# Optimization experiments

Hardware: AMD Instinct MI355X
Metric: run time of the kernel (lower is better)

The kernel has to match this reference:

```python
import jax, jax.numpy as jnp
import numpy as np

N_USERS = 60000
N_ITEMS = 40000
D = 64
N_BEH = 3
L_GLOBAL = 2
L_SINGLE = 2
E_GLOBAL = 1_000_000
E_BEH = 500_000
BATCH = 4096
REG_WEIGHT = 1e-3
DIM_QK = 64
N_NODES = N_USERS + 1 + N_ITEMS + 1
USER_GLOBAL_W = 2.35
USER_BEH_W = 0.242
ITEM_GLOBAL_W = 1.0
ITEM_BEH_W = 0.55


def setup_inputs() -> dict:
    key = jax.random.key(0)
    ks = jax.random.split(key, 9)
    user_emb = (jax.random.normal(ks[0], (N_USERS + 1, D), jnp.float32) * 0.1).at[0].set(0.0)
    item_emb = (jax.random.normal(ks[1], (N_ITEMS + 1, D), jnp.float32) * 0.1).at[0].set(0.0)
    w_scale = 1.0 / np.sqrt(D)
    global_W = jax.random.normal(ks[2], (L_GLOBAL, D, D), jnp.float32) * w_scale
    global_b = jnp.zeros((L_GLOBAL, D), jnp.float32)
    beh_W = jax.random.normal(ks[3], (N_BEH, L_SINGLE, D, D), jnp.float32) * w_scale
    beh_b = jnp.zeros((N_BEH, L_SINGLE, D), jnp.float32)
    all_edge_index = jax.random.randint(ks[4], (2, E_GLOBAL), 0, N_NODES, jnp.int32)
    beh_edge_index = jax.random.randint(ks[5], (N_BEH, 2, E_BEH), 0, N_NODES, jnp.int32)
    batch_data = jax.random.randint(ks[6], (BATCH, N_BEH, 3), 0, N_ITEMS + 1, jnp.int32)
    return {
        "user_emb": user_emb, "item_emb": item_emb,
        "global_W": global_W, "global_b": global_b,
        "beh_W": beh_W, "beh_b": beh_b,
        "all_edge_index": all_edge_index, "beh_edge_index": beh_edge_index,
        "batch_data": batch_data,
    }


def _gcn_conv(h, src, dst, W, b):
    # PyG GCNConv, add_self_loops=False: out[dst] += d^-1/2[src] d^-1/2[dst] (h W)[src] + b
    N = h.shape[0]
    hw = h @ W
    deg = jnp.zeros((N,), hw.dtype).at[dst].add(1.0)
    dinv = jnp.where(deg > 0, jax.lax.rsqrt(jnp.maximum(deg, 1.0)), 0.0)
    coef = (dinv[src] * dinv[dst])[:, None]          # [E,1]
    out = jax.ops.segment_sum(hw[src] * coef, dst, num_segments=N)
    return out + b


def _graph_encoder(x, edge_index, Ws, bs):
    src, dst = edge_index[0], edge_index[1]
    res = x
    h = x
    for i in range(Ws.shape[0]):
        h = _gcn_conv(h, src, dst, Ws[i], bs[i])
        h = h / jnp.maximum(jnp.linalg.norm(h, axis=-1, keepdims=True), 1e-12)  # F.normalize
        res = res + h / (i + 1.0)
    return res


def _mutual_attention(tok):
    # tok: [N, B, D]; per-node BxB softmax attention
    scale = 1.0 / np.sqrt(DIM_QK)
    att = jax.nn.softmax(jnp.einsum('nbd,ncd->nbc', tok, tok) * scale, axis=-1)
    return jnp.einsum('nbc,ncd->nbd', att, tok)


def reference(user_emb, item_emb, global_W, global_b, beh_W, beh_b,
              all_edge_index, beh_edge_index, batch_data):
    nu = user_emb.shape[0]
    all_emb = jnp.concatenate([user_emb, item_emb], axis=0)        # [N, D]
    all_emb = _graph_encoder(all_emb, all_edge_index, global_W, global_b)
    u_g, i_g = all_emb[:nu], all_emb[nu:]
    beh_u, beh_i = [], []
    for b_idx in range(N_BEH):
        e = _graph_encoder(all_emb, beh_edge_index[b_idx], beh_W[b_idx], beh_b[b_idx])
        beh_u.append(e[:nu])
        beh_i.append(e[nu:])
    all_u = jnp.stack(beh_u, axis=1)                               # [nu, B, D]
    all_i = jnp.stack(beh_i, axis=1)                               # [ni, B, D]
    all_u = _mutual_attention(all_u)
    all_i = _mutual_attention(all_i)
    uw = USER_GLOBAL_W * u_g[:, None, :] + USER_BEH_W * all_u      # [nu, B, D]
    iw = ITEM_GLOBAL_W * i_g[:, None, :] + ITEM_BEH_W * all_i      # [ni, B, D]

    total = jnp.float32(0.0)
    for i in range(N_BEH):
        data = batch_data[:, i]
        users = data[:, 0]
        items = data[:, 1:]                                        # [batch, 2]
        uf = uw[:, i][users][:, None, :]                           # [batch, 1, D]
        for j in range(N_BEH):
            itf = iw[:, j][items]                                  # [batch, 2, D]
            scores = jnp.sum(uf * itf, axis=2)                     # [batch, 2]
            total = total - jnp.mean(jax.nn.log_sigmoid(scores[:, 0] - scores[:, 1]))
    emb_loss = (jnp.linalg.norm(user_emb) + jnp.linalg.norm(item_emb)) / item_emb.shape[0]
    return total + REG_WEIGHT * emb_loss
```

## Files before the change

### kernel.cpp

```cpp
#include <hip/hip_runtime.h>
#include <math.h>

#define NU 60001
#define NI 40001
#define NN 100002
#define EG 1000000
#define EB 500000
#define BATCH 4096
#define NPASS 4
#define PASSW 25001
#define EC 36
#define SENTB (NN * 64)

typedef float floatx2 __attribute__((ext_vector_type(2)));
typedef short bf16x8 __attribute__((ext_vector_type(8)));
typedef float f32x4 __attribute__((ext_vector_type(4)));

__device__ inline float wave_sum(float v) {
#pragma unroll
  for (int off = 32; off > 0; off >>= 1) v += __shfl_down(v, off);
  return __shfl(v, 0);
}

__device__ inline float sub_sum16(float v) {
#pragma unroll
  for (int off = 8; off > 0; off >>= 1) v += __shfl_xor(v, off);
  return v;
}

__device__ inline float dot4(float4 a, float4 b) {
  return fmaf(a.x, b.x, fmaf(a.y, b.y, fmaf(a.z, b.z, a.w * b.w)));
}

__device__ inline unsigned short f2b(float f) {
  unsigned u = __float_as_uint(f);
  return (unsigned short)((u + 0x7fffu + ((u >> 16) & 1u)) >> 16);
}
__device__ inline float b2f(unsigned short h) {
  return __uint_as_float((unsigned)h << 16);
}
__device__ inline float4 ld4b(const unsigned short* p) {
  ushort4 u = *(const ushort4*)p;
  return make_float4(b2f(u.x), b2f(u.y), b2f(u.z), b2f(u.w));
}
__device__ inline unsigned pack2b(float a, float b) {
  return (unsigned)f2b(a) | ((unsigned)f2b(b) << 16);
}

__device__ inline unsigned char f2fp8(float f) {
  return (unsigned char)(__builtin_amdgcn_cvt_pk_fp8_f32(f, f, 0, false) & 0xff);
}
__device__ inline unsigned int pack4_fp8(float4 v) {
  int pk = __builtin_amdgcn_cvt_pk_fp8_f32(v.x, v.y, 0, false);
  pk = __builtin_amdgcn_cvt_pk_fp8_f32(v.z, v.w, pk, true);
  return (unsigned int)pk;
}

__global__ void k_bucket(const int* __restrict__ eg, const int* __restrict__ eb,
                         int* __restrict__ cnt, int* __restrict__ edg,
                         int lo, int hi) {
  int set = blockIdx.y;
  int E = set ? EB : EG;
  int e = blockIdx.x * blockDim.x + threadIdx.x;
  if (e >= E) return;
  const int* sp = set ? (eb + (long)(set - 1) * 2 * EB) : eg;
  int d = sp[E + e];
  if (d < lo || d >= hi) return;
  int s = sp[e];
  int pos = atomicAdd(cnt + set * NN + d, 1);
  if (pos < EC) edg[((long)set * NN + d) * EC + pos] = s << 6;
}

__global__ void k_dinv(const int* __restrict__ cnt, float* __restrict__ dinv) {
  int i = blockIdx.x * blockDim.x + threadIdx.x;
  if (i < 4 * NN) {
    int c = cnt[i];
    dinv[i] = (c > 0) ? rsqrtf((float)c) : 0.f;
  }
}

__global__ void k_prepw(const float* __restrict__ gW, const float* __restrict__ bW,
                        unsigned short* __restrict__ wt) {
  int t = blockIdx.x * blockDim.x + threadIdx.x;
  if (t >= 8 * 4096) return;
  int m = t >> 12, idx = t & 4095;
  int col = idx >> 6, k = idx & 63;
  const float* src = (m < 2) ? (gW + m * 4096) : (bW + (long)(m - 2) * 4096);
  wt[t] = f2b(src[k * 64 + col]);
}

__global__ void k_zsent(unsigned char* __restrict__ tbsb, unsigned char* __restrict__ asg,
                        unsigned char* __restrict__ asb) {
  const long NEp = (long)(NN + 1) * 64;
  int t = threadIdx.x;
  int row = t >> 6, b = t & 63;
  if (row < 3) tbsb[row * NEp + SENTB + b] = 0;
  else if (row == 3) asg[SENTB + b] = 0;
  else if (row < 7) asb[(row - 4) * NEp + SENTB + b] = 0;
}

__global__ void k_tbs0(const float4* __restrict__ ue, const float4* __restrict__ ie,
                       const float* __restrict__ dinv, unsigned int* __restrict__ out) {
  long i = (long)blockIdx.x * blockDim.x + threadIdx.x;
  if (i >= (long)(NN + 1) * 16) return;
  int row = (int)(i >> 4);
  if (row >= NN) { out[i] = 0; return; }
  float4 v = (row < NU) ? ue[i] : ie[i - (long)NU * 16];
  float dv = dinv[row];
  v.x *= dv; v.y *= dv; v.z *= dv; v.w *= dv;
  out[i] = pack4_fp8(v);
}

#define CVT8(r)                                       \
  a0 += __builtin_amdgcn_cvt_pk_f32_fp8(r.x, false);  \
  a1 += __builtin_amdgcn_cvt_pk_f32_fp8(r.x, true);   \
  a2 += __builtin_amdgcn_cvt_pk_f32_fp8(r.y, false);  \
  a3 += __builtin_amdgcn_cvt_pk_f32_fp8(r.y, true);

template <int MODE>
__global__ void __launch_bounds__(256) k_gcn(
    const unsigned char* __restrict__ tb, const int* __restrict__ edg,
    const int* __restrict__ cnt, const float* __restrict__ dinv,
    const unsigned short* __restrict__ Wt, const float* __restrict__ biasb,
    const float* __restrict__ basef, const float* __restrict__ base2f,
    const unsigned short* __restrict__ base16,
    unsigned short* __restrict__ res16, unsigned char* __restrict__ outS,
    unsigned char* __restrict__ tbs123) {
  __shared__ __align__(16) short accs[32][72];
  __shared__ float ssq[32][2];
  const long NE = (long)NN * 64;
  const long NEp = (long)(NN + 1) * 64;

  int t = threadIdx.x;
  int w = t >> 6, lane = t & 63;
  int sub3 = lane >> 3, sl8 = lane & 7;
  int sub = lane >> 4, sl16 = lane & 15;
  int set = blockIdx.y;

  const float* bias;
  if (MODE <= 1) bias = biasb;
  else bias = biasb + set * 128 + (MODE == 3 ? 64 : 0);
  const unsigned short* wt = Wt + ((MODE >= 2) ? (long)set * 8192 : 0);
  int cs = (MODE >= 2) ? (1 + set) : 0;
  const unsigned char* tbl = (MODE >= 2) ? tb + (long)set * NEp : tb;
  unsigned char* outp = (MODE == 2) ? outS + (long)set * NEp : outS;

  int tilebase = (w >> 1) << 4;
  int cg = (w & 1) << 5;
  int ncolA = cg + sl16, ncolB = cg + 16 + sl16;
  bf16x8 bfA0 = *(const bf16x8*)(wt + ncolA * 64 + (sub << 3));
  bf16x8 bfA1 = *(const bf16x8*)(wt + ncolA * 64 + 32 + (sub << 3));
  bf16x8 bfB0 = *(const bf16x8*)(wt + ncolB * 64 + (sub << 3));
  bf16x8 bfB1 = *(const bf16x8*)(wt + ncolB * 64 + 32 + (sub << 3));
  float biasA = bias[ncolA], biasB = bias[ncolB];

  int nb0 = blockIdx.x * 32;
  int node = nb0 + (w << 3) + sub3;
  floatx2 a0 = {0.f, 0.f}, a1 = {0.f, 0.f}, a2 = {0.f, 0.f}, a3 = {0.f, 0.f};
  int deg = 0;
  float dvn = 0.f;
  const int* ep = edg;
  if (node < NN) {
    deg = min(cnt[cs * NN + node], EC);
    dvn = dinv[cs * NN + node];
    ep = edg + ((long)cs * NN + node) * EC;
  }
  int mx = deg;
  mx = max(mx, __shfl_xor(mx, 8));
  mx = max(mx, __shfl_xor(mx, 16));
  mx = max(mx, __shfl_xor(mx, 32));
  for (int ch = 0; ch < mx; ch += 8) {
    int rem = deg - ch;
#pragma unroll
    for (int i = 0; i < 8; i += 4) {
      int s0 = ep[ch + i + 0];
      int s1 = ep[ch + i + 1];
      int s2 = ep[ch + i + 2];
      int s3 = ep[ch + i + 3];
      int o0 = (i + 0 < rem) ? s0 : SENTB;
      int o1 = (i + 1 < rem) ? s1 : SENTB;
      int o2 = (i + 2 < rem) ? s2 : SENTB;
      int o3 = (i + 3 < rem) ? s3 : SENTB;
      uint2 r0 = *(const uint2*)(tbl + o0 + (sl8 << 3));
      uint2 r1 = *(const uint2*)(tbl + o1 + (sl8 << 3));
      uint2 r2 = *(const uint2*)(tbl + o2 + (sl8 << 3));
      uint2 r3 = *(const uint2*)(tbl + o3 + (sl8 << 3));
      CVT8(r0); CVT8(r1); CVT8(r2); CVT8(r3);
    }
  }
  floatx2 dv2 = {dvn, dvn};
  a0 *= dv2; a1 *= dv2; a2 *= dv2; a3 *= dv2;
  int4 pk4;
  pk4.x = (int)pack2b(a0.x, a0.y);
  pk4.y = (int)pack2b(a1.x, a1.y);
  pk4.z = (int)pack2b(a2.x, a2.y);
  pk4.w = (int)pack2b(a3.x, a3.y);
  *(int4*)&accs[(w << 3) + sub3][sl8 << 3] = pk4;
  __syncthreads();

  int arow = tilebase + sl16;
  bf16x8 fa0 = *(const bf16x8*)&accs[arow][sub << 3];
  bf16x8 fa1 = *(const bf16x8*)&accs[arow][32 + (sub << 3)];
  f32x4 cA = {0.f, 0.f, 0.f, 0.f}, cB = {0.f, 0.f, 0.f, 0.f};
  cA = __builtin_amdgcn_mfma_f32_16x16x32_bf16(fa0, bfA0, cA, 0, 0, 0);
  cA = __builtin_amdgcn_mfma_f32_16x16x32_bf16(fa1, bfA1, cA, 0, 0, 0);
  cB = __builtin_amdgcn_mfma_f32_16x16x32_bf16(fa0, bfB0, cB, 0, 0, 0);
  cB = __builtin_amdgcn_mfma_f32_16x16x32_bf16(fa1, bfB1, cB, 0, 0, 0);

  float vA[4], vB[4];
#pragma unroll
  for (int r = 0; r < 4; r++) { vA[r] = cA[r] + biasA; vB[r] = cB[r] + biasB; }
#pragma unroll
  for (int r = 0; r < 4; r++) {
    float p = sub_sum16(fmaf(vA[r], vA[r], vB[r] * vB[r]));
    if (sl16 == 0) ssq[tilebase + (sub << 2) + r][w & 1] = p;
  }
  __syncthreads();
#pragma unroll
  for (int r = 0; r < 4; r++) {
    int nl = tilebase + (sub << 2) + r;
    float ss = ssq[nl][0] + ssq[nl][1];
    float inv = 1.0f / fmaxf(sqrtf(ss), 1e-12f);
    float hA = vA[r] * inv, hB = vB[r] * inv;
    int gn = nb0 + nl;
    if (gn < NN) {
      long iA = (long)gn * 64 + ncolA, iB = (long)gn * 64 + ncolB;
      float dv = dinv[cs * NN + gn];
      if (MODE == 0 || MODE == 2) {
        outp[iA] = f2fp8(hA * dv);
        outp[iB] = f2fp8(hB * dv);
      } else if (MODE == 1) {
        float idv = (dv > 0.f) ? 1.0f / dv : 0.f;
        float ownA = __builtin_amdgcn_cvt_f32_fp8((unsigned int)tbl[iA], 0) * idv;
        float ownB = __builtin_amdgcn_cvt_f32_fp8((unsigned int)tbl[iB], 0) * idv;
        float bA, bB;
        if (gn < NU) { bA = basef[iA]; bB = basef[iB]; }
        else {
          long o2 = (long)(gn - NU) * 64;
          bA = base2f[o2 + ncolA]; bB = base2f[o2 + ncolB];
        }
        float rA = bA + ownA + 0.5f * hA, rB = bB + ownB + 0.5f * hB;
        res16[iA] = f2b(rA); res16[iB] = f2b(rB);
#pragma unroll
        for (int k = 0; k < 3; k++) {
          float dk = dinv[(1 + k) * NN + gn];
          tbs123[(long)k * NEp + iA] = f2fp8(rA * dk);
          tbs123[(long)k * NEp + iB] = f2fp8(rB * dk);
        }
      } else {
        float idv = (dv > 0.f) ? 1.0f / dv : 0.f;
        float ownA = __builtin_amdgcn_cvt_f32_fp8((unsigned int)tbl[iA], 0) * idv;
        float ownB = __builtin_amdgcn_cvt_f32_fp8((unsigned int)tbl[iB], 0) * idv;
        float rA = b2f(base16[iA]) + ownA + 0.5f * hA;
        float rB = b2f(base16[iB]) + ownB + 0.5f * hB;
        (res16 + (long)set * NE)[iA] = f2b(rA);
        (res16 + (long)set * NE)[iB] = f2b(rB);
      }
    }
  }
}

__device__ inline void item_iw4(const unsigned short* __restrict__ G,
                                const unsigned short* __restrict__ B0,
                                const unsigned short* __restrict__ B1,
                                const unsigned short* __restrict__ B2,
                                long o, float4& iw0, float4& iw1, float4& iw2) {
  float4 g = ld4b(G + o);
  float4 t0 = ld4b(B0 + o);
  float4 t1 = ld4b(B1 + o);
  float4 t2 = ld4b(B2 + o);
  float g00 = sub_sum16(dot4(t0, t0)), g01 = sub_sum16(dot4(t0, t1));
  float g02 = sub_sum16(dot4(t0, t2)), g11 = sub_sum16(dot4(t1, t1));
  float g12 = sub_sum16(dot4(t1, t2)), g22 = sub_sum16(dot4(t2, t2));
  const float S = 0.125f;
  float gm[3][3] = {{g00, g01, g02}, {g01, g11, g12}, {g02, g12, g22}};
  float4* out[3] = {&iw0, &iw1, &iw2};
#pragma unroll
  for (int j = 0; j < 3; j++) {
    float a0 = gm[j][0] * S, a1 = gm[j][1] * S, a2 = gm[j][2] * S;
    float m = fmaxf(a0, fmaxf(a1, a2));
    float e0 = expf(a0 - m), e1 = expf(a1 - m), e2 = expf(a2 - m);
    float inv = 1.f / (e0 + e1 + e2);
    float w0 = e0 * inv, w1 = e1 * inv, w2 = e2 * inv;
    float4 r;
    r.x = fmaf(0.55f, w0 * t0.x + w1 * t1.x + w2 * t2.x, g.x);
    r.y = fmaf(0.55f, w0 * t0.y + w1 * t1.y + w2 * t2.y, g.y);
    r.z = fmaf(0.55f, w0 * t0.z + w1 * t1.z + w2 * t2.z, g.z);
    r.w = fmaf(0.55f, w0 * t0.w + w1 * t1.w + w2 * t2.w, g.w);
    *out[j] = r;
  }
}

__global__ void __launch_bounds__(256) k_loss(
    const unsigned short* __restrict__ G, const unsigned short* __restrict__ B0,
    const unsigned short* __restrict__ B1, const unsigned short* __restrict__ B2,
    const int* __restrict__ batch, float* __restrict__ acc) {
  int tid = blockIdx.x * blockDim.x + threadIdx.x;
  int lane = tid & 63;
  int sub = lane >> 4, sl = lane & 15;
  int task = (tid >> 6) * 4 + sub;
  if (task >= BATCH * 3) return;
  int i = task % 3;
  const int* bd = batch + (long)task * 3;
  int u = bd[0], p = bd[1], q = bd[2];

  float4 uf;
  {
    long o = (long)u * 64 + sl * 4;
    float4 g = ld4b(G + o);
    float4 t0 = ld4b(B0 + o);
    float4 t1 = ld4b(B1 + o);
    float4 t2 = ld4b(B2 + o);
    float4 ti = (i == 0) ? t0 : ((i == 1) ? t1 : t2);
    float a0 = sub_sum16(dot4(ti, t0)) * 0.125f;
    float a1 = sub_sum16(dot4(ti, t1)) * 0.125f;
    float a2 = sub_sum16(dot4(ti, t2)) * 0.125f;
    float m = fmaxf(a0, fmaxf(a1, a2));
    float e0 = expf(a0 - m), e1 = expf(a1 - m), e2 = expf(a2 - m);
    float inv = 1.f / (e0 + e1 + e2);
    float w0 = e0 * inv, w1 = e1 * inv, w2 = e2 * inv;
    uf.x = fmaf(2.35f, g.x, 0.242f * (w0 * t0.x + w1 * t1.x + w2 * t2.x));
    uf.y = fmaf(2.35f, g.y, 0.242f * (w0 * t0.y + w1 * t1.y + w2 * t2.y));
    uf.z = fmaf(2.35f, g.z, 0.242f * (w0 * t0.z + w1 * t1.z + w2 * t2.z));
    uf.w = fmaf(2.35f, g.w, 0.242f * (w0 * t0.w + w1 * t1.w + w2 * t2.w));
  }

  float4 p0, p1, p2, q0, q1, q2;
  item_iw4(G, B0, B1, B2, ((long)(NU + p)) * 64 + sl * 4, p0, p1, p2);
  item_iw4(G, B0, B1, B2, ((long)(NU + q)) * 64 + sl * 4, q0, q1, q2);

  float sp0 = sub_sum16(dot4(uf, p0)), sq0 = sub_sum16(dot4(uf, q0));
  float sp1 = sub_sum16(dot4(uf, p1)), sq1 = sub_sum16(dot4(uf, q1));
  float sp2 = sub_sum16(dot4(uf, p2)), sq2 = sub_sum16(dot4(uf, q2));

  if (sl == 0) {
    float loc = 0.f;
    float xs[3] = {sp0 - sq0, sp1 - sq1, sp2 - sq2};
#pragma unroll
    for (int j = 0; j < 3; j++) {
      float x = xs[j];
      loc += fminf(x, 0.f) - log1pf(expf(-fabsf(x)));
    }
    atomicAdd(acc, loc);
  }
}

__global__ void k_sumsq(const float* __restrict__ x, long n, float* __restrict__ acc) {
  long stride = (long)gridDim.x * blockDim.x;
  float v = 0.f;
  for (long i = (long)blockIdx.x * blockDim.x + threadIdx.x; i < n; i += stride) {
    float t = x[i];
    v = fmaf(t, t, v);
  }
  v = wave_sum(v);
  if ((threadIdx.x & 63) == 0) atomicAdd(acc, v);
}

__global__ void k_final(const float* __restrict__ acc, float* __restrict__ out) {
  out[0] = -acc[0] * (1.0f / (float)BATCH) +
           0.001f * ((sqrtf(acc[1]) + sqrtf(acc[2])) / (float)NI);
}

extern "C" void kernel_launch(void* const* d_in, const int* in_sizes, int n_in,
                              void* d_out, int out_size, void* d_ws, size_t ws_size,
                              hipStream_t stream) {
  const float* ue = (const float*)d_in[0];
  const float* ie = (const float*)d_in[1];
  const float* gW = (const float*)d_in[2];
  const float* gb = (const float*)d_in[3];
  const float* bW = (const float*)d_in[4];
  const float* bb = (const float*)d_in[5];
  const int* eg = (const int*)d_in[6];
  const int* eb = (const int*)d_in[7];
  const int* batch = (const int*)d_in[8];
  float* out = (float*)d_out;

  const long NE = (long)NN * 64;
  const long NEp = (long)(NN + 1) * 64;
  unsigned short* G16 = (unsigned short*)d_ws;
  unsigned short* B16 = G16 + NE;
  float* DINV = (float*)(B16 + 3 * NE);
  float* ACC = DINV + 4 * NN;
  int* CNT = (int*)(ACC + 8);
  unsigned short* WT = (unsigned short*)(CNT + 4 * NN);
  int* EDG = (int*)(WT + 8 * 4096);
  unsigned char* TBS0 = (unsigned char*)(EDG + 4L * NN * EC);
  unsigned char* TBSb = TBS0 + NEp;
  unsigned char* ASg = TBSb + 3 * NEp;
  unsigned char* ASb = ASg + NEp;

  hipMemsetAsync(ACC, 0, 8 * sizeof(float), stream);
  hipMemsetAsync(CNT, 0, 4 * NN * sizeof(int), stream);

  const int GB = (NN + 31) / 32;

  dim3 ge((EG + 255) / 256, 4);

  for (int p = 0; p < NPASS; p++)
    k_bucket<<<ge, 256, 0, stream>>>(eg, eb, CNT, EDG,
                                     p * PASSW, min(NN, (p + 1) * PASSW));
  k_dinv<<<(4 * NN + 255) / 256, 256, 0, stream>>>(CNT, DINV);

  k_prepw<<<128, 256, 0, stream>>>(gW, bW, WT);

  k_zsent<<<1, 512, 0, stream>>>(TBSb, ASg, ASb);
  k_tbs0<<<(int)(((NN + 1) * 16 + 255) / 256), 256, 0, stream>>>(
      (const float4*)ue, (const float4*)ie, DINV, (unsigned int*)TBS0);

  k_gcn<0><<<dim3(GB, 1), 256, 0, stream>>>(TBS0, EDG, CNT, DINV, WT, gb,
                                            nullptr, nullptr, nullptr, nullptr,
                                            ASg, nullptr);
  k_gcn<1><<<dim3(GB, 1), 256, 0, stream>>>(ASg, EDG, CNT, DINV, WT + 4096,
                                            gb + 64, ue, ie, nullptr, G16,
                                            nullptr, TBSb);

  k_gcn<2><<<dim3(GB, 3), 256, 0, stream>>>(TBSb, EDG, CNT, DINV, WT + 8192,
                                            bb, nullptr, nullptr, nullptr,
                                            nullptr, ASb, nullptr);
  k_gcn<3><<<dim3(GB, 3), 256, 0, stream>>>(ASb, EDG, CNT, DINV, WT + 12288,
                                            bb, nullptr, nullptr, G16, B16,
                                            nullptr, nullptr);

  k_loss<<<(BATCH * 3) / 16, 256, 0, stream>>>(G16, B16, B16 + NE, B16 + 2 * NE,
                                               batch, ACC);

  k_sumsq<<<512, 256, 0, stream>>>(ue, (long)NU * 64, ACC + 1);
  k_sumsq<<<512, 256, 0, stream>>>(ie, (long)NI * 64, ACC + 2);

  k_final<<<1, 1, 0, stream>>>(ACC, out);
}
```

Measured before the change: 533.9 us.

## Prefetch first 16 edges per node, split accumulators, fuse prep kernels

Merges the dinv, weight-prep and sentinel-zeroing kernels into one launch. The GCN gather kernel now loads the first 16 edge indices as int4 vectors and issues 16 independent neighbour gathers at once, with two accumulator sets to raise memory-level parallelism. Weight and bias fragment loads move after the gather to ease register pressure, and launch bounds now request 8 blocks per CU. Nodes with low degree still pay for the 16 sentinel loads, and the occupancy hint may cause register spills.

```diff
diff --git a/kernel.cpp b/kernel.cpp
--- a/kernel.cpp
+++ b/kernel.cpp
@@ -71,32 +71,29 @@
   if (pos < EC) edg[((long)set * NN + d) * EC + pos] = s << 6;
 }
 
-__global__ void k_dinv(const int* __restrict__ cnt, float* __restrict__ dinv) {
+__global__ void k_prep(const int* __restrict__ cnt, float* __restrict__ dinv,
+                       const float* __restrict__ gW, const float* __restrict__ bW,
+                       unsigned short* __restrict__ wt,
+                       unsigned char* __restrict__ tbsb, unsigned char* __restrict__ asg,
+                       unsigned char* __restrict__ asb) {
+  const long NEp = (long)(NN + 1) * 64;
   int i = blockIdx.x * blockDim.x + threadIdx.x;
   if (i < 4 * NN) {
     int c = cnt[i];
     dinv[i] = (c > 0) ? rsqrtf((float)c) : 0.f;
   }
-}
-
-__global__ void k_prepw(const float* __restrict__ gW, const float* __restrict__ bW,
-                        unsigned short* __restrict__ wt) {
-  int t = blockIdx.x * blockDim.x + threadIdx.x;
-  if (t >= 8 * 4096) return;
-  int m = t >> 12, idx = t & 4095;
-  int col = idx >> 6, k = idx & 63;
-  const float* src = (m < 2) ? (gW + m * 4096) : (bW + (long)(m - 2) * 4096);
-  wt[t] = f2b(src[k * 64 + col]);
-}
-
-__global__ void k_zsent(unsigned char* __restrict__ tbsb, unsigned char* __restrict__ asg,
-                        unsigned char* __restrict__ asb) {
-  const long NEp = (long)(NN + 1) * 64;
-  int t = threadIdx.x;
-  int row = t >> 6, b = t & 63;
-  if (row < 3) tbsb[row * NEp + SENTB + b] = 0;
-  else if (row == 3) asg[SENTB + b] = 0;
-  else if (row < 7) asb[(row - 4) * NEp + SENTB + b] = 0;
+  if (i < 8 * 4096) {
+    int m = i >> 12, idx = i & 4095;
+    int col = idx >> 6, k = idx & 63;
+    const float* src = (m < 2) ? (gW + m * 4096) : (bW + (long)(m - 2) * 4096);
+    wt[i] = f2b(src[k * 64 + col]);
+  }
+  if (i < 448) {
+    int row = i >> 6, b = i & 63;
+    if (row < 3) tbsb[row * NEp + SENTB + b] = 0;
+    else if (row == 3) asg[SENTB + b] = 0;
+    else asb[(row - 4) * NEp + SENTB + b] = 0;
+  }
 }
 
 __global__ void k_tbs0(const float4* __restrict__ ue, const float4* __restrict__ ie,
@@ -111,14 +108,20 @@
   out[i] = pack4_fp8(v);
 }
 
-#define CVT8(r)                                       \
+#define CVTA(r)                                       \
   a0 += __builtin_amdgcn_cvt_pk_f32_fp8(r.x, false);  \
   a1 += __builtin_amdgcn_cvt_pk_f32_fp8(r.x, true);   \
   a2 += __builtin_amdgcn_cvt_pk_f32_fp8(r.y, false);  \
   a3 += __builtin_amdgcn_cvt_pk_f32_fp8(r.y, true);
 
+#define CVTB(r)                                       \
+  b0 += __builtin_amdgcn_cvt_pk_f32_fp8(r.x, false);  \
+  b1 += __builtin_amdgcn_cvt_pk_f32_fp8(r.x, true);   \
+  b2 += __builtin_amdgcn_cvt_pk_f32_fp8(r.y, false);  \
+  b3 += __builtin_amdgcn_cvt_pk_f32_fp8(r.y, true);
+
 template <int MODE>
-__global__ void __launch_bounds__(256) k_gcn(
+__global__ void __launch_bounds__(256, 8) k_gcn(
     const unsigned char* __restrict__ tb, const int* __restrict__ edg,
     const int* __restrict__ cnt, const float* __restrict__ dinv,
     const unsigned short* __restrict__ Wt, const float* __restrict__ biasb,
@@ -148,46 +151,87 @@
   int tilebase = (w >> 1) << 4;
   int cg = (w & 1) << 5;
   int ncolA = cg + sl16, ncolB = cg + 16 + sl16;
-  bf16x8 bfA0 = *(const bf16x8*)(wt + ncolA * 64 + (sub << 3));
-  bf16x8 bfA1 = *(const bf16x8*)(wt + ncolA * 64 + 32 + (sub << 3));
-  bf16x8 bfB0 = *(const bf16x8*)(wt + ncolB * 64 + (sub << 3));
-  bf16x8 bfB1 = *(const bf16x8*)(wt + ncolB * 64 + 32 + (sub << 3));
-  float biasA = bias[ncolA], biasB = bias[ncolB];
 
   int nb0 = blockIdx.x * 32;
   int node = nb0 + (w << 3) + sub3;
-  floatx2 a0 = {0.f, 0.f}, a1 = {0.f, 0.f}, a2 = {0.f, 0.f}, a3 = {0.f, 0.f};
-  int deg = 0;
-  float dvn = 0.f;
-  const int* ep = edg;
-  if (node < NN) {
-    deg = min(cnt[cs * NN + node], EC);
-    dvn = dinv[cs * NN + node];
-    ep = edg + ((long)cs * NN + node) * EC;
-  }
+  bool vn = node < NN;
+  const int* ep = edg + ((long)cs * NN + (vn ? node : 0)) * EC;
+  int4 e0 = *(const int4*)(ep);
+  int4 e1 = *(const int4*)(ep + 4);
+  int4 e2 = *(const int4*)(ep + 8);
+  int4 e3 = *(const int4*)(ep + 12);
+  int deg = vn ? min(cnt[cs * NN + node], EC) : 0;
+  float dvn = vn ? dinv[cs * NN + node] : 0.f;
   int mx = deg;
   mx = max(mx, __shfl_xor(mx, 8));
   mx = max(mx, __shfl_xor(mx, 16));
   mx = max(mx, __shfl_xor(mx, 32));
-  for (int ch = 0; ch < mx; ch += 8) {
+
+  int ls = sl8 << 3;
+  floatx2 a0 = {0.f, 0.f}, a1 = {0.f, 0.f}, a2 = {0.f, 0.f}, a3 = {0.f, 0.f};
+  floatx2 b0 = {0.f, 0.f}, b1 = {0.f, 0.f}, b2 = {0.f, 0.f}, b3 = {0.f, 0.f};
+  {
+    int o0 = (0 < deg) ? e0.x : SENTB;
+    int o1 = (1 < deg) ? e0.y : SENTB;
+    int o2 = (2 < deg) ? e0.z : SENTB;
+    int o3 = (3 < deg) ? e0.w : SENTB;
+    int o4 = (4 < deg) ? e1.x : SENTB;
+    int o5 = (5 < deg) ? e1.y : SENTB;
+    int o6 = (6 < deg) ? e1.z : SENTB;
+    int o7 = (7 < deg) ? e1.w : SENTB;
+    int o8 = (8 < deg) ? e2.x : SENTB;
+    int o9 = (9 < deg) ? e2.y : SENTB;
+    int o10 = (10 < deg) ? e2.z : SENTB;
+    int o11 = (11 < deg) ? e2.w : SENTB;
+    int o12 = (12 < deg) ? e3.x : SENTB;
+    int o13 = (13 < deg) ? e3.y : SENTB;
+    int o14 = (14 < deg) ? e3.z : SENTB;
+    int o15 = (15 < deg) ? e3.w : SENTB;
+    uint2 r0 = *(const uint2*)(tbl + o0 + ls);
+    uint2 r1 = *(const uint2*)(tbl + o1 + ls);
+    uint2 r2 = *(const uint2*)(tbl + o2 + ls);
+    uint2 r3 = *(const uint2*)(tbl + o3 + ls);
+    uint2 r4 = *(const uint2*)(tbl + o4 + ls);
+    uint2 r5 = *(const uint2*)(tbl + o5 + ls);
+    uint2 r6 = *(const uint2*)(tbl + o6 + ls);
+    uint2 r7 = *(const uint2*)(tbl + o7 + ls);
+    uint2 r8 = *(const uint2*)(tbl + o8 + ls);
+    uint2 r9 = *(const uint2*)(tbl + o9 + ls);
+    uint2 r10 = *(const uint2*)(tbl + o10 + ls);
+    uint2 r11 = *(const uint2*)(tbl + o11 + ls);
+    uint2 r12 = *(const uint2*)(tbl + o12 + ls);
+    uint2 r13 = *(const uint2*)(tbl + o13 + ls);
+    uint2 r14 = *(const uint2*)(tbl + o14 + ls);
+    uint2 r15 = *(const uint2*)(tbl + o15 + ls);
+    CVTA(r0); CVTA(r1); CVTA(r2); CVTA(r3);
+    CVTA(r4); CVTA(r5); CVTA(r6); CVTA(r7);
+    CVTB(r8); CVTB(r9); CVTB(r10); CVTB(r11);
+    CVTB(r12); CVTB(r13); CVTB(r14); CVTB(r15);
+  }
+  for (int ch = 16; ch < mx; ch += 8) {
     int rem = deg - ch;
-#pragma unroll
-    for (int i = 0; i < 8; i += 4) {
-      int s0 = ep[ch + i + 0];
-      int s1 = ep[ch + i + 1];
-      int s2 = ep[ch + i + 2];
-      int s3 = ep[ch + i + 3];
-      int o0 = (i + 0 < rem) ? s0 : SENTB;
-      int o1 = (i + 1 < rem) ? s1 : SENTB;
-      int o2 = (i + 2 < rem) ? s2 : SENTB;
-      int o3 = (i + 3 < rem) ? s3 : SENTB;
-      uint2 r0 = *(const uint2*)(tbl + o0 + (sl8 << 3));
-      uint2 r1 = *(const uint2*)(tbl + o1 + (sl8 << 3));
-      uint2 r2 = *(const uint2*)(tbl + o2 + (sl8 << 3));
-      uint2 r3 = *(const uint2*)(tbl + o3 + (sl8 << 3));
-      CVT8(r0); CVT8(r1); CVT8(r2); CVT8(r3);
-    }
-  }
+    int4 f0 = *(const int4*)(ep + ch);
+    int4 f1 = *(const int4*)(ep + ch + 4);
+    int o0 = (0 < rem) ? f0.x : SENTB;
+    int o1 = (1 < rem) ? f0.y : SENTB;
+    int o2 = (2 < rem) ? f0.z : SENTB;
+    int o3 = (3 < rem) ? f0.w : SENTB;
+    int o4 = (4 < rem) ? f1.x : SENTB;
+    int o5 = (5 < rem) ? f1.y : SENTB;
+    int o6 = (6 < rem) ? f1.z : SENTB;
+    int o7 = (7 < rem) ? f1.w : SENTB;
+    uint2 r0 = *(const uint2*)(tbl + o0 + ls);
+    uint2 r1 = *(const uint2*)(tbl + o1 + ls);
+    uint2 r2 = *(const uint2*)(tbl + o2 + ls);
+    uint2 r3 = *(const uint2*)(tbl + o3 + ls);
+    uint2 r4 = *(const uint2*)(tbl + o4 + ls);
+    uint2 r5 = *(const uint2*)(tbl + o5 + ls);
+    uint2 r6 = *(const uint2*)(tbl + o6 + ls);
+    uint2 r7 = *(const uint2*)(tbl + o7 + ls);
+    CVTA(r0); CVTA(r1); CVTA(r2); CVTA(r3);
+    CVTB(r4); CVTB(r5); CVTB(r6); CVTB(r7);
+  }
+  a0 += b0; a1 += b1; a2 += b2; a3 += b3;
   floatx2 dv2 = {dvn, dvn};
   a0 *= dv2; a1 *= dv2; a2 *= dv2; a3 *= dv2;
   int4 pk4;
@@ -196,6 +240,12 @@
   pk4.z = (int)pack2b(a2.x, a2.y);
   pk4.w = (int)pack2b(a3.x, a3.y);
   *(int4*)&accs[(w << 3) + sub3][sl8 << 3] = pk4;
+
+  bf16x8 bfA0 = *(const bf16x8*)(wt + ncolA * 64 + (sub << 3));
+  bf16x8 bfA1 = *(const bf16x8*)(wt + ncolA * 64 + 32 + (sub << 3));
+  bf16x8 bfB0 = *(const bf16x8*)(wt + ncolB * 64 + (sub << 3));
+  bf16x8 bfB1 = *(const bf16x8*)(wt + ncolB * 64 + 32 + (sub << 3));
+  float biasA = bias[ncolA], biasB = bias[ncolB];
   __syncthreads();
 
   int arow = tilebase + sl16;
@@ -399,11 +449,9 @@
   for (int p = 0; p < NPASS; p++)
     k_bucket<<<ge, 256, 0, stream>>>(eg, eb, CNT, EDG,
                                      p * PASSW, min(NN, (p + 1) * PASSW));
-  k_dinv<<<(4 * NN + 255) / 256, 256, 0, stream>>>(CNT, DINV);
-
-  k_prepw<<<128, 256, 0, stream>>>(gW, bW, WT);
-
-  k_zsent<<<1, 512, 0, stream>>>(TBSb, ASg, ASb);
+
+  k_prep<<<(4 * NN + 255) / 256, 256, 0, stream>>>(CNT, DINV, gW, bW, WT,
+                                                   TBSb, ASg, ASb);
   k_tbs0<<<(int)(((NN + 1) * 16 + 255) / 256), 256, 0, stream>>>(
       (const float4*)ue, (const float4*)ie, DINV, (unsigned int*)TBS0);
 
```

After: 523.6 us. No clear change (-1.9%).
